# Optimization experiments

Hardware: AMD Instinct MI355X
Metric: run time of the kernel (lower is better)

Reference implementation:

```python
import jax, jax.numpy as jnp
import numpy as np

PRESERVE_RATIO = 0.8
TEMPERATURE = 1.5


def setup_inputs() -> dict:
    key = jax.random.key(0)
    ks = jax.random.split(key, 8)
    B, C, H, W = 2, 64, 96, 96
    inter = C // 2
    bott = C // 4
    s = 0.02
    return {
        "x": jax.random.normal(ks[0], (B, C, H, W), dtype=jnp.float32),
        "g_w": jax.random.normal(ks[1], (inter, C), dtype=jnp.float32) * s,
        "theta_w": jax.random.normal(ks[2], (inter, C), dtype=jnp.float32) * s,
        "phi_w": jax.random.normal(ks[3], (inter, C), dtype=jnp.float32) * s,
        "W_w": jax.random.normal(ks[4], (C, inter), dtype=jnp.float32) * s,
        "cg1_w": jax.random.normal(ks[5], (bott, C), dtype=jnp.float32) * s,
        "cg1_b": jnp.zeros((bott,), dtype=jnp.float32),
        "cg2_w": jax.random.normal(ks[6], (C, bott), dtype=jnp.float32) * s,
        "cg2_b": jnp.zeros((C,), dtype=jnp.float32),
    }


def reference(x, g_w, theta_w, phi_w, W_w, cg1_w, cg1_b, cg2_w, cg2_b):
    B, C, H, W = x.shape
    N = H * W
    # color gate: global avg pool -> 1x1 conv -> relu -> 1x1 conv -> sigmoid
    pooled = jnp.mean(x, axis=(2, 3))                       # [B, C]
    h = jax.nn.relu(pooled @ cg1_w.T + cg1_b)               # [B, C//4]
    gate = jax.nn.sigmoid(h @ cg2_w.T + cg2_b)              # [B, C]

    xf = x.reshape(B, C, N)                                 # [B, C, N]
    g_x = jnp.einsum('ic,bcn->bni', g_w, xf)                # [B, N, I]
    theta = jnp.einsum('ic,bcn->bni', theta_w, xf)          # [B, N, I]
    phi = jnp.einsum('ic,bcn->bin', phi_w, xf)              # [B, I, N]

    affinity = jnp.einsum('bni,bim->bnm', theta, phi) / TEMPERATURE  # [B, N, N]
    affinity = jax.nn.softmax(affinity, axis=-1)
    y = jnp.einsum('bnm,bmi->bni', affinity, g_x)           # [B, N, I]
    y = jnp.einsum('ci,bni->bcn', W_w, y).reshape(B, C, H, W)
    y = y * gate[:, :, None, None] * PRESERVE_RATIO
    return x + y
```

## Files before the change

kernel.cpp:

```cpp
#include <hip/hip_runtime.h>

#define N_TOK 9216
#define C_DIM 64
#define I_DIM 32
#define BOT 16
#define B_SZ 2
#define N_TILES 144

typedef short bf16x8 __attribute__((ext_vector_type(8)));
typedef float f32x4 __attribute__((ext_vector_type(4)));
typedef float f32x16 __attribute__((ext_vector_type(16)));

#define KST 40
#define VST 72

__device__ __forceinline__ unsigned packbf(float a, float b) {
  return __builtin_amdgcn_perm(__float_as_uint(b), __float_as_uint(a), 0x07060302u);
}
__device__ __forceinline__ unsigned short bftrunc(float f) {
  return (unsigned short)(__float_as_uint(f) >> 16);
}
__device__ __forceinline__ float bflo(unsigned u) { return __uint_as_float(u << 16); }
__device__ __forceinline__ float bfhi(unsigned u) { return __uint_as_float(u & 0xffff0000u); }

__global__ __launch_bounds__(256) void proj_pool_kernel(
    const float* __restrict__ x, const float* __restrict__ g_w,
    const float* __restrict__ theta_w, const float* __restrict__ phi_w,
    unsigned short* __restrict__ Q, unsigned short* __restrict__ K,
    unsigned short* __restrict__ VT, float* __restrict__ pooled) {
  if (blockIdx.x >= 216) {
    int bc = blockIdx.x - 216;
    const float* p = x + (size_t)bc * N_TOK;
    float s = 0.f;
    for (int t = threadIdx.x; t < N_TOK; t += 256) s += p[t];
#pragma unroll
    for (int off = 32; off >= 1; off >>= 1) s += __shfl_down(s, off, 64);
    __shared__ float red[4];
    int wid = threadIdx.x >> 6, lane = threadIdx.x & 63;
    if (lane == 0) red[wid] = s;
    __syncthreads();
    if (threadIdx.x == 0)
      pooled[bc] = (red[0] + red[1] + red[2] + red[3]) * (1.0f / N_TOK);
    return;
  }
  const int lane = threadIdx.x & 63;
  const int m = lane & 15, quad = lane >> 4;
  int task = blockIdx.x * 4 + (threadIdx.x >> 6);
  int mat = task / 288;
  int r0 = task % 288;
  int b = r0 / 144;
  int n0 = (r0 % 144) * 64;
  const float* wsrc = (mat == 0) ? theta_w : ((mat == 1) ? phi_w : g_w);
  const float scale = (mat == 0) ? 0.96179669439f : 1.0f;

  bf16x8 afr[2][2];
#pragma unroll
  for (int it = 0; it < 2; ++it)
#pragma unroll
    for (int cs = 0; cs < 2; ++cs) {
      const float* wp = wsrc + (it * 16 + m) * C_DIM + cs * 32 + quad * 8;
      union { unsigned u[4]; bf16x8 v; } t;
#pragma unroll
      for (int j = 0; j < 4; ++j)
        t.u[j] = packbf(wp[2 * j] * scale, wp[2 * j + 1] * scale);
      afr[it][cs] = t.v;
    }

#pragma unroll
  for (int sub = 0; sub < 4; ++sub) {
    const int ns = n0 + sub * 16;
    const float* xb = x + (size_t)b * C_DIM * N_TOK + ns + m;
    bf16x8 bfr[2];
#pragma unroll
    for (int cs = 0; cs < 2; ++cs) {
      union { unsigned u[4]; bf16x8 v; } t;
#pragma unroll
      for (int j = 0; j < 4; ++j) {
        float v0 = xb[(size_t)(cs * 32 + quad * 8 + 2 * j) * N_TOK];
        float v1 = xb[(size_t)(cs * 32 + quad * 8 + 2 * j + 1) * N_TOK];
        t.u[j] = packbf(v0, v1);
      }
      bfr[cs] = t.v;
    }

    f32x4 acc[2] = {{0.f, 0.f, 0.f, 0.f}, {0.f, 0.f, 0.f, 0.f}};
#pragma unroll
    for (int cs = 0; cs < 2; ++cs)
#pragma unroll
      for (int it = 0; it < 2; ++it)
        acc[it] = __builtin_amdgcn_mfma_f32_16x16x32_bf16(afr[it][cs], bfr[cs],
                                                          acc[it], 0, 0, 0);
    if (mat < 2) {
      unsigned short* dst =
          ((mat == 0) ? Q : K) + ((size_t)b * N_TOK + ns + m) * I_DIM;
#pragma unroll
      for (int it = 0; it < 2; ++it) {
        unsigned u0 = packbf(acc[it][0], acc[it][1]);
        unsigned u1 = packbf(acc[it][2], acc[it][3]);
        *(uint2*)(dst + it * 16 + quad * 4) = make_uint2(u0, u1);
      }
    } else {
#pragma unroll
      for (int it = 0; it < 2; ++it)
#pragma unroll
        for (int r = 0; r < 4; ++r)
          VT[((size_t)b * I_DIM + it * 16 + quad * 4 + r) * N_TOK + ns + m] =
              bftrunc(acc[it][r]);
    }
  }
}

__device__ __forceinline__ void tilework(const f32x16 s, const bf16x8 bvA,
                                         const bf16x8 bvB, f32x16& accy,
                                         float& lsum) {
  float e[16];
#pragma unroll
  for (int r = 0; r < 16; ++r) e[r] = __builtin_amdgcn_exp2f(s[r]);
  float l0 = 0.f, l1 = 0.f, l2 = 0.f, l3 = 0.f;
#pragma unroll
  for (int r = 0; r < 4; ++r) {
    l0 += e[r]; l1 += e[4 + r]; l2 += e[8 + r]; l3 += e[12 + r];
  }
  lsum += (l0 + l1) + (l2 + l3);
  unsigned pk[8];
#pragma unroll
  for (int i = 0; i < 8; ++i) pk[i] = packbf(e[2 * i], e[2 * i + 1]);
  asm("v_permlane32_swap_b32 %0, %1" : "+v"(pk[0]), "+v"(pk[2]));
  asm("v_permlane32_swap_b32 %0, %1" : "+v"(pk[1]), "+v"(pk[3]));
  asm("v_permlane32_swap_b32 %0, %1" : "+v"(pk[4]), "+v"(pk[6]));
  asm("v_permlane32_swap_b32 %0, %1" : "+v"(pk[5]), "+v"(pk[7]));
  union { unsigned u[4]; bf16x8 v; } A0, A1;
  A0.u[0] = pk[0]; A0.u[1] = pk[1]; A0.u[2] = pk[2]; A0.u[3] = pk[3];
  A1.u[0] = pk[4]; A1.u[1] = pk[5]; A1.u[2] = pk[6]; A1.u[3] = pk[7];
  accy = __builtin_amdgcn_mfma_f32_32x32x16_bf16(A0.v, bvA, accy, 0, 0, 0);
  accy = __builtin_amdgcn_mfma_f32_32x32x16_bf16(A1.v, bvB, accy, 0, 0, 0);
}

__global__ __launch_bounds__(256, 4) void attn_kernel(
    const unsigned short* __restrict__ Q, const unsigned short* __restrict__ Kg,
    const unsigned short* __restrict__ VT, unsigned short* __restrict__ Ypart,
    float* __restrict__ Lpart, int tps) {
  const int tid = threadIdx.x;
  const int lane = tid & 63;
  const int l32 = lane & 31, h = lane >> 5;
  const int ks = blockIdx.y, b = blockIdx.z;
  const int q0 = blockIdx.x * 128 + (tid >> 6) * 32;
  const unsigned short* Qb = Q + (size_t)b * N_TOK * I_DIM;
  const unsigned short* Kb = Kg + (size_t)b * N_TOK * I_DIM;
  const unsigned short* Vb = VT + (size_t)b * I_DIM * N_TOK;

  __shared__ __align__(16) unsigned short Ks[2][64 * KST];
  __shared__ __align__(16) unsigned short Vs[2][32 * VST];

  bf16x8 bq0 = *(const bf16x8*)(Qb + (size_t)(q0 + l32) * I_DIM + h * 8);
  bf16x8 bq1 = *(const bf16x8*)(Qb + (size_t)(q0 + l32) * I_DIM + 16 + h * 8);

  f32x16 accy = {};
  float lsum = 0.f;
  const f32x16 zz = {};

  const int kt0 = ks * tps;
  const int kr = tid >> 2, kc = (tid & 3) * 8;
  const int vr = tid >> 3, vc = (tid & 7) * 8;
  const unsigned short* kgp = Kb + ((size_t)kt0 * 64 + kr) * I_DIM + kc;
  const unsigned short* vgp = Vb + (size_t)vr * N_TOK + kt0 * 64 + vc;

  {
    uint4 r0k = *(const uint4*)kgp;
    uint4 r0v = *(const uint4*)vgp;
    *(uint4*)&Ks[0][kr * KST + kc] = r0k;
    *(uint4*)&Vs[0][vr * VST + vc] = r0v;
  }
  uint4 rk = {0, 0, 0, 0}, rv = {0, 0, 0, 0};
  if (tps > 1) {
    rk = *(const uint4*)(kgp + 64 * I_DIM);
    rv = *(const uint4*)(vgp + 64);
  }
  __syncthreads();

  for (int kt = 0; kt < tps; ++kt) {
    const int p = kt & 1;
    uint4 rk2 = {0, 0, 0, 0}, rv2 = {0, 0, 0, 0};
    if (kt + 2 < tps) {
      rk2 = *(const uint4*)(kgp + (size_t)(kt + 2) * 64 * I_DIM);
      rv2 = *(const uint4*)(vgp + (kt + 2) * 64);
    }
    asm volatile("" ::: "memory");

    bf16x8 ak00 = *(const bf16x8*)&Ks[p][l32 * KST + 8 * h];
    bf16x8 ak01 = *(const bf16x8*)&Ks[p][l32 * KST + 16 + 8 * h];
    bf16x8 ak10 = *(const bf16x8*)&Ks[p][(32 + l32) * KST + 8 * h];
    bf16x8 ak11 = *(const bf16x8*)&Ks[p][(32 + l32) * KST + 16 + 8 * h];
    bf16x8 bv0 = *(const bf16x8*)&Vs[p][l32 * VST + 8 * h];
    bf16x8 bv1 = *(const bf16x8*)&Vs[p][l32 * VST + 16 + 8 * h];
    bf16x8 bv2 = *(const bf16x8*)&Vs[p][l32 * VST + 32 + 8 * h];
    bf16x8 bv3 = *(const bf16x8*)&Vs[p][l32 * VST + 48 + 8 * h];

    f32x16 s0 = __builtin_amdgcn_mfma_f32_32x32x16_bf16(ak00, bq0, zz, 0, 0, 0);
    s0 = __builtin_amdgcn_mfma_f32_32x32x16_bf16(ak01, bq1, s0, 0, 0, 0);
    f32x16 s1 = __builtin_amdgcn_mfma_f32_32x32x16_bf16(ak10, bq0, zz, 0, 0, 0);
    s1 = __builtin_amdgcn_mfma_f32_32x32x16_bf16(ak11, bq1, s1, 0, 0, 0);

    tilework(s0, bv0, bv1, accy, lsum);
    tilework(s1, bv2, bv3, accy, lsum);

    if (kt + 1 < tps) {
      *(uint4*)&Ks[1 - p][kr * KST + kc] = rk;
      *(uint4*)&Vs[1 - p][vr * VST + vc] = rv;
    }
    rk = rk2; rv = rv2;
    __syncthreads();
  }

  lsum += __shfl_xor(lsum, 32, 64);

  const size_t base = (size_t)(ks * B_SZ + b) * N_TOK + q0;
#pragma unroll
  for (int R = 0; R < 4; ++R)
#pragma unroll
    for (int r = 0; r < 4; ++r)
      Ypart[(base + r + 8 * R + 4 * h) * I_DIM + l32] = bftrunc(accy[4 * R + r]);
  if (h == 0) Lpart[base + l32] = lsum;
}

__global__ __launch_bounds__(256) void epilogue_kernel(
    const float* __restrict__ x, const float* __restrict__ W_w,
    const float* __restrict__ pooled, const float* __restrict__ cg1_w,
    const float* __restrict__ cg1_b, const float* __restrict__ cg2_w,
    const float* __restrict__ cg2_b, const unsigned short* __restrict__ Ypart,
    const float* __restrict__ Lpart, float* __restrict__ out, int KS) {
  __shared__ float Ysh[64][33];
  __shared__ float lsh[64];
  __shared__ float gsh[64];
  __shared__ float hl[BOT];
  const int t = threadIdx.x;
  const int b = blockIdx.y;
  const int n0 = blockIdx.x * 64;

  if (t < BOT) {
    float a = cg1_b[t];
#pragma unroll
    for (int c = 0; c < C_DIM; ++c)
      a += cg1_w[t * C_DIM + c] * pooled[b * C_DIM + c];
    hl[t] = a > 0.f ? a : 0.f;
  }

  {
    int nl = t >> 2, i0 = (t & 3) * 8;
    float s[8];
#pragma unroll
    for (int k = 0; k < 8; ++k) s[k] = 0.f;
    for (int ks = 0; ks < KS; ++ks) {
      const unsigned short* yp =
          Ypart + ((size_t)(ks * B_SZ + b) * N_TOK + n0 + nl) * I_DIM + i0;
      uint4 v = *(const uint4*)yp;
      s[0] += bflo(v.x); s[1] += bfhi(v.x);
      s[2] += bflo(v.y); s[3] += bfhi(v.y);
      s[4] += bflo(v.z); s[5] += bfhi(v.z);
      s[6] += bflo(v.w); s[7] += bfhi(v.w);
    }
#pragma unroll
    for (int k = 0; k < 8; ++k) Ysh[nl][i0 + k] = s[k];
    if (t < 64) {
      float ls = 0.f;
      for (int ks = 0; ks < KS; ++ks)
        ls += Lpart[(size_t)(ks * B_SZ + b) * N_TOK + n0 + t];
      lsh[t] = ls;
    }
  }
  __syncthreads();

  if (t < C_DIM) {
    float z = cg2_b[t];
#pragma unroll
    for (int j = 0; j < BOT; ++j) z += cg2_w[t * BOT + j] * hl[j];
    gsh[t] = 0.8f / (1.f + __expf(-z));
  }
  __syncthreads();

  const int n = t & 63, cg = t >> 6;
  float y[I_DIM];
#pragma unroll
  for (int i = 0; i < I_DIM; ++i) y[i] = Ysh[n][i];
  const float inv = 1.0f / lsh[n];
  const float* xb = x + ((size_t)b * C_DIM + cg * 16) * N_TOK + n0 + n;
  float* ob = out + ((size_t)b * C_DIM + cg * 16) * N_TOK + n0 + n;
#pragma unroll
  for (int c16 = 0; c16 < 16; ++c16) {
    const int c = cg * 16 + c16;
    float sacc = 0.f;
#pragma unroll
    for (int i = 0; i < I_DIM; ++i) sacc += W_w[c * I_DIM + i] * y[i];
    ob[(size_t)c16 * N_TOK] = xb[(size_t)c16 * N_TOK] + gsh[c] * inv * sacc;
  }
}

extern "C" void kernel_launch(void* const* d_in, const int* in_sizes, int n_in,
                              void* d_out, int out_size, void* d_ws, size_t ws_size,
                              hipStream_t stream) {
  const float* x = (const float*)d_in[0];
  const float* g_w = (const float*)d_in[1];
  const float* theta_w = (const float*)d_in[2];
  const float* phi_w = (const float*)d_in[3];
  const float* W_w = (const float*)d_in[4];
  const float* cg1_w = (const float*)d_in[5];
  const float* cg1_b = (const float*)d_in[6];
  const float* cg2_w = (const float*)d_in[7];
  const float* cg2_b = (const float*)d_in[8];
  float* out = (float*)d_out;

  char* w = (char*)d_ws;
  const size_t bfsz = (size_t)B_SZ * N_TOK * I_DIM * sizeof(unsigned short);
  unsigned short* Qb = (unsigned short*)(w);
  unsigned short* Kb = (unsigned short*)(w + bfsz);
  unsigned short* VT = (unsigned short*)(w + 2 * bfsz);
  float* pooled = (float*)(w + 3 * bfsz);
  char* w2 = w + 3 * bfsz + 8192;

  int KS = 16;
  {
    const size_t per = (size_t)B_SZ * N_TOK * (I_DIM * 2 + 4);
    while (KS > 1 && (3 * bfsz + 8192 + (size_t)KS * per) > ws_size) KS >>= 1;
  }
  float* Lpart = (float*)w2;
  unsigned short* Ypart =
      (unsigned short*)(w2 + (size_t)KS * B_SZ * N_TOK * sizeof(float));
  int tps = N_TILES / KS;

  proj_pool_kernel<<<dim3(344), 256, 0, stream>>>(x, g_w, theta_w, phi_w, Qb,
                                                  Kb, VT, pooled);
  attn_kernel<<<dim3(72, KS, B_SZ), 256, 0, stream>>>(Qb, Kb, VT, Ypart, Lpart, tps);
  epilogue_kernel<<<dim3(N_TOK / 64, B_SZ), 256, 0, stream>>>(
      x, W_w, pooled, cg1_w, cg1_b, cg2_w, cg2_b, Ypart, Lpart, out, KS);
}
```

Before: 147.0 us.

## Process two query groups per wave and single-buffer K/V tiles

Each wave now handles 64 queries (two 32-row groups) instead of 32, so every K/V tile loaded into shared memory and registers is reused across twice as many MFMA score/PV computations. Blocks shrink to 128 threads (2 waves), and the double-buffered shared tiles become single-buffered, with prefetch held in registers and two barriers per iteration. This lowers LDS traffic per query, but costs more registers (two accumulators, four Q fragments), lowers occupancy and adds a barrier per iteration.

```diff
diff --git a/kernel.cpp b/kernel.cpp
--- a/kernel.cpp
+++ b/kernel.cpp
@@ -136,7 +136,7 @@
   accy = __builtin_amdgcn_mfma_f32_32x32x16_bf16(A1.v, bvB, accy, 0, 0, 0);
 }
 
-__global__ __launch_bounds__(256, 4) void attn_kernel(
+__global__ __launch_bounds__(128, 2) void attn_kernel(
     const unsigned short* __restrict__ Q, const unsigned short* __restrict__ Kg,
     const unsigned short* __restrict__ VT, unsigned short* __restrict__ Ypart,
     float* __restrict__ Lpart, int tps) {
@@ -144,83 +144,101 @@
   const int lane = tid & 63;
   const int l32 = lane & 31, h = lane >> 5;
   const int ks = blockIdx.y, b = blockIdx.z;
-  const int q0 = blockIdx.x * 128 + (tid >> 6) * 32;
+  const int q0 = blockIdx.x * 128 + (tid >> 6) * 64;
   const unsigned short* Qb = Q + (size_t)b * N_TOK * I_DIM;
   const unsigned short* Kb = Kg + (size_t)b * N_TOK * I_DIM;
   const unsigned short* Vb = VT + (size_t)b * I_DIM * N_TOK;
 
-  __shared__ __align__(16) unsigned short Ks[2][64 * KST];
-  __shared__ __align__(16) unsigned short Vs[2][32 * VST];
-
-  bf16x8 bq0 = *(const bf16x8*)(Qb + (size_t)(q0 + l32) * I_DIM + h * 8);
-  bf16x8 bq1 = *(const bf16x8*)(Qb + (size_t)(q0 + l32) * I_DIM + 16 + h * 8);
-
-  f32x16 accy = {};
-  float lsum = 0.f;
+  __shared__ __align__(16) unsigned short Ks[64 * KST];
+  __shared__ __align__(16) unsigned short Vs[32 * VST];
+
+  bf16x8 bq[4];
+#pragma unroll
+  for (int qg = 0; qg < 2; ++qg) {
+    bq[2 * qg] = *(const bf16x8*)(Qb + (size_t)(q0 + qg * 32 + l32) * I_DIM + h * 8);
+    bq[2 * qg + 1] =
+        *(const bf16x8*)(Qb + (size_t)(q0 + qg * 32 + l32) * I_DIM + 16 + h * 8);
+  }
+
+  f32x16 accy[2] = {{}, {}};
+  float lsum[2] = {0.f, 0.f};
   const f32x16 zz = {};
 
   const int kt0 = ks * tps;
-  const int kr = tid >> 2, kc = (tid & 3) * 8;
-  const int vr = tid >> 3, vc = (tid & 7) * 8;
+  const int kr = tid >> 1, kc = (tid & 1) * 16;
+  const int vr = tid >> 2, vc = (tid & 3) * 16;
   const unsigned short* kgp = Kb + ((size_t)kt0 * 64 + kr) * I_DIM + kc;
   const unsigned short* vgp = Vb + (size_t)vr * N_TOK + kt0 * 64 + vc;
+  unsigned short* klp = &Ks[kr * KST + kc];
+  unsigned short* vlp = &Vs[vr * VST + vc];
 
   {
-    uint4 r0k = *(const uint4*)kgp;
-    uint4 r0v = *(const uint4*)vgp;
-    *(uint4*)&Ks[0][kr * KST + kc] = r0k;
-    *(uint4*)&Vs[0][vr * VST + vc] = r0v;
-  }
-  uint4 rk = {0, 0, 0, 0}, rv = {0, 0, 0, 0};
-  if (tps > 1) {
-    rk = *(const uint4*)(kgp + 64 * I_DIM);
-    rv = *(const uint4*)(vgp + 64);
-  }
-  __syncthreads();
+    uint4 k0a = *(const uint4*)kgp;
+    uint4 k0b = *(const uint4*)(kgp + 8);
+    uint4 v0a = *(const uint4*)vgp;
+    uint4 v0b = *(const uint4*)(vgp + 8);
+    *(uint4*)(klp) = k0a;
+    *(uint4*)(klp + 8) = k0b;
+    *(uint4*)(vlp) = v0a;
+    *(uint4*)(vlp + 8) = v0b;
+  }
 
   for (int kt = 0; kt < tps; ++kt) {
-    const int p = kt & 1;
-    uint4 rk2 = {0, 0, 0, 0}, rv2 = {0, 0, 0, 0};
-    if (kt + 2 < tps) {
-      rk2 = *(const uint4*)(kgp + (size_t)(kt + 2) * 64 * I_DIM);
-      rv2 = *(const uint4*)(vgp + (kt + 2) * 64);
+    __syncthreads();
+    const bool pf = (kt + 1 < tps);
+    uint4 rka = {0, 0, 0, 0}, rkb = rka, rva = rka, rvb = rka;
+    if (pf) {
+      const unsigned short* kn = kgp + (size_t)(kt + 1) * 64 * I_DIM;
+      const unsigned short* vn = vgp + (kt + 1) * 64;
+      rka = *(const uint4*)kn;
+      rkb = *(const uint4*)(kn + 8);
+      rva = *(const uint4*)vn;
+      rvb = *(const uint4*)(vn + 8);
     }
     asm volatile("" ::: "memory");
 
-    bf16x8 ak00 = *(const bf16x8*)&Ks[p][l32 * KST + 8 * h];
-    bf16x8 ak01 = *(const bf16x8*)&Ks[p][l32 * KST + 16 + 8 * h];
-    bf16x8 ak10 = *(const bf16x8*)&Ks[p][(32 + l32) * KST + 8 * h];
-    bf16x8 ak11 = *(const bf16x8*)&Ks[p][(32 + l32) * KST + 16 + 8 * h];
-    bf16x8 bv0 = *(const bf16x8*)&Vs[p][l32 * VST + 8 * h];
-    bf16x8 bv1 = *(const bf16x8*)&Vs[p][l32 * VST + 16 + 8 * h];
-    bf16x8 bv2 = *(const bf16x8*)&Vs[p][l32 * VST + 32 + 8 * h];
-    bf16x8 bv3 = *(const bf16x8*)&Vs[p][l32 * VST + 48 + 8 * h];
-
-    f32x16 s0 = __builtin_amdgcn_mfma_f32_32x32x16_bf16(ak00, bq0, zz, 0, 0, 0);
-    s0 = __builtin_amdgcn_mfma_f32_32x32x16_bf16(ak01, bq1, s0, 0, 0, 0);
-    f32x16 s1 = __builtin_amdgcn_mfma_f32_32x32x16_bf16(ak10, bq0, zz, 0, 0, 0);
-    s1 = __builtin_amdgcn_mfma_f32_32x32x16_bf16(ak11, bq1, s1, 0, 0, 0);
-
-    tilework(s0, bv0, bv1, accy, lsum);
-    tilework(s1, bv2, bv3, accy, lsum);
-
-    if (kt + 1 < tps) {
-      *(uint4*)&Ks[1 - p][kr * KST + kc] = rk;
-      *(uint4*)&Vs[1 - p][vr * VST + vc] = rv;
-    }
-    rk = rk2; rv = rv2;
+    bf16x8 ak00 = *(const bf16x8*)&Ks[l32 * KST + 8 * h];
+    bf16x8 ak01 = *(const bf16x8*)&Ks[l32 * KST + 16 + 8 * h];
+    bf16x8 ak10 = *(const bf16x8*)&Ks[(32 + l32) * KST + 8 * h];
+    bf16x8 ak11 = *(const bf16x8*)&Ks[(32 + l32) * KST + 16 + 8 * h];
+    bf16x8 bv0 = *(const bf16x8*)&Vs[l32 * VST + 8 * h];
+    bf16x8 bv1 = *(const bf16x8*)&Vs[l32 * VST + 16 + 8 * h];
+    bf16x8 bv2 = *(const bf16x8*)&Vs[l32 * VST + 32 + 8 * h];
+    bf16x8 bv3 = *(const bf16x8*)&Vs[l32 * VST + 48 + 8 * h];
+
+#pragma unroll
+    for (int qg = 0; qg < 2; ++qg) {
+      f32x16 s0 = __builtin_amdgcn_mfma_f32_32x32x16_bf16(ak00, bq[2 * qg], zz, 0, 0, 0);
+      s0 = __builtin_amdgcn_mfma_f32_32x32x16_bf16(ak01, bq[2 * qg + 1], s0, 0, 0, 0);
+      f32x16 s1 = __builtin_amdgcn_mfma_f32_32x32x16_bf16(ak10, bq[2 * qg], zz, 0, 0, 0);
+      s1 = __builtin_amdgcn_mfma_f32_32x32x16_bf16(ak11, bq[2 * qg + 1], s1, 0, 0, 0);
+      tilework(s0, bv0, bv1, accy[qg], lsum[qg]);
+      tilework(s1, bv2, bv3, accy[qg], lsum[qg]);
+    }
+
     __syncthreads();
-  }
-
-  lsum += __shfl_xor(lsum, 32, 64);
+    if (pf) {
+      *(uint4*)(klp) = rka;
+      *(uint4*)(klp + 8) = rkb;
+      *(uint4*)(vlp) = rva;
+      *(uint4*)(vlp + 8) = rvb;
+    }
+  }
+
+#pragma unroll
+  for (int qg = 0; qg < 2; ++qg) lsum[qg] += __shfl_xor(lsum[qg], 32, 64);
 
   const size_t base = (size_t)(ks * B_SZ + b) * N_TOK + q0;
 #pragma unroll
-  for (int R = 0; R < 4; ++R)
-#pragma unroll
-    for (int r = 0; r < 4; ++r)
-      Ypart[(base + r + 8 * R + 4 * h) * I_DIM + l32] = bftrunc(accy[4 * R + r]);
-  if (h == 0) Lpart[base + l32] = lsum;
+  for (int qg = 0; qg < 2; ++qg) {
+#pragma unroll
+    for (int R = 0; R < 4; ++R)
+#pragma unroll
+      for (int r = 0; r < 4; ++r)
+        Ypart[(base + qg * 32 + r + 8 * R + 4 * h) * I_DIM + l32] =
+            bftrunc(accy[qg][4 * R + r]);
+    if (h == 0) Lpart[base + qg * 32 + l32] = lsum[qg];
+  }
 }
 
 __global__ __launch_bounds__(256) void epilogue_kernel(
@@ -329,7 +347,7 @@
 
   proj_pool_kernel<<<dim3(344), 256, 0, stream>>>(x, g_w, theta_w, phi_w, Qb,
                                                   Kb, VT, pooled);
-  attn_kernel<<<dim3(72, KS, B_SZ), 256, 0, stream>>>(Qb, Kb, VT, Ypart, Lpart, tps);
+  attn_kernel<<<dim3(72, KS, B_SZ), 128, 0, stream>>>(Qb, Kb, VT, Ypart, Lpart, tps);
   epilogue_kernel<<<dim3(N_TOK / 64, B_SZ), 256, 0, stream>>>(
       x, W_w, pooled, cg1_w, cg1_b, cg2_w, cg2_b, Ypart, Lpart, out, KS);
 }
```

Result: slower. 150.2 us (+2.2%).

## Fuse epilogue into attention via last-block counter, merge QKV projections, single-buffer LDS

Applied to the files above, without the earlier changes.

The epilogue kernel is removed. Its work now runs inside the attention kernel: the last key-split block to finish for each query tile, detected through an atomic counter that the projection kernel zeroes, does the reduction. The projection kernel now computes theta, phi and g together per task, so x is read once instead of three times, and it launches fewer blocks. The attention K/V staging changes from double-buffered LDS to a single buffer with register prefetch and two barriers per tile, which saves shared memory but may expose more latency. The aim is to cut one launch and repeated x reads, at the cost of serialized tail work in the last blocks.

```diff
diff --git a/kernel.cpp b/kernel.cpp
--- a/kernel.cpp
+++ b/kernel.cpp
@@ -27,9 +27,10 @@
     const float* __restrict__ x, const float* __restrict__ g_w,
     const float* __restrict__ theta_w, const float* __restrict__ phi_w,
     unsigned short* __restrict__ Q, unsigned short* __restrict__ K,
-    unsigned short* __restrict__ VT, float* __restrict__ pooled) {
-  if (blockIdx.x >= 216) {
-    int bc = blockIdx.x - 216;
+    unsigned short* __restrict__ VT, float* __restrict__ pooled,
+    int* __restrict__ cnt) {
+  if (blockIdx.x >= 72) {
+    int bc = blockIdx.x - 72;
     const float* p = x + (size_t)bc * N_TOK;
     float s = 0.f;
     for (int t = threadIdx.x; t < N_TOK; t += 256) s += p[t];
@@ -43,28 +44,31 @@
       pooled[bc] = (red[0] + red[1] + red[2] + red[3]) * (1.0f / N_TOK);
     return;
   }
+  if (blockIdx.x == 0 && threadIdx.x < 72 * B_SZ) cnt[threadIdx.x] = 0;
+
   const int lane = threadIdx.x & 63;
   const int m = lane & 15, quad = lane >> 4;
   int task = blockIdx.x * 4 + (threadIdx.x >> 6);
-  int mat = task / 288;
-  int r0 = task % 288;
-  int b = r0 / 144;
-  int n0 = (r0 % 144) * 64;
-  const float* wsrc = (mat == 0) ? theta_w : ((mat == 1) ? phi_w : g_w);
-  const float scale = (mat == 0) ? 0.96179669439f : 1.0f;
-
-  bf16x8 afr[2][2];
-#pragma unroll
-  for (int it = 0; it < 2; ++it)
-#pragma unroll
-    for (int cs = 0; cs < 2; ++cs) {
-      const float* wp = wsrc + (it * 16 + m) * C_DIM + cs * 32 + quad * 8;
-      union { unsigned u[4]; bf16x8 v; } t;
-#pragma unroll
-      for (int j = 0; j < 4; ++j)
-        t.u[j] = packbf(wp[2 * j] * scale, wp[2 * j + 1] * scale);
-      afr[it][cs] = t.v;
-    }
+  int b = task / 144;
+  int n0 = (task % 144) * 64;
+
+  bf16x8 afr[3][2][2];
+#pragma unroll
+  for (int m3 = 0; m3 < 3; ++m3) {
+    const float* wsrc = (m3 == 0) ? theta_w : ((m3 == 1) ? phi_w : g_w);
+    const float scale = (m3 == 0) ? 0.96179669439f : 1.0f;
+#pragma unroll
+    for (int it = 0; it < 2; ++it)
+#pragma unroll
+      for (int cs = 0; cs < 2; ++cs) {
+        const float* wp = wsrc + (it * 16 + m) * C_DIM + cs * 32 + quad * 8;
+        union { unsigned u[4]; bf16x8 v; } t;
+#pragma unroll
+        for (int j = 0; j < 4; ++j)
+          t.u[j] = packbf(wp[2 * j] * scale, wp[2 * j + 1] * scale);
+        afr[m3][it][cs] = t.v;
+      }
+  }
 
 #pragma unroll
   for (int sub = 0; sub < 4; ++sub) {
@@ -83,30 +87,37 @@
       bfr[cs] = t.v;
     }
 
-    f32x4 acc[2] = {{0.f, 0.f, 0.f, 0.f}, {0.f, 0.f, 0.f, 0.f}};
+    f32x4 acc[3][2];
+#pragma unroll
+    for (int m3 = 0; m3 < 3; ++m3)
+#pragma unroll
+      for (int it = 0; it < 2; ++it) acc[m3][it] = (f32x4){0.f, 0.f, 0.f, 0.f};
 #pragma unroll
     for (int cs = 0; cs < 2; ++cs)
 #pragma unroll
-      for (int it = 0; it < 2; ++it)
-        acc[it] = __builtin_amdgcn_mfma_f32_16x16x32_bf16(afr[it][cs], bfr[cs],
-                                                          acc[it], 0, 0, 0);
-    if (mat < 2) {
+      for (int m3 = 0; m3 < 3; ++m3)
+#pragma unroll
+        for (int it = 0; it < 2; ++it)
+          acc[m3][it] = __builtin_amdgcn_mfma_f32_16x16x32_bf16(
+              afr[m3][it][cs], bfr[cs], acc[m3][it], 0, 0, 0);
+
+#pragma unroll
+    for (int m3 = 0; m3 < 2; ++m3) {
       unsigned short* dst =
-          ((mat == 0) ? Q : K) + ((size_t)b * N_TOK + ns + m) * I_DIM;
+          ((m3 == 0) ? Q : K) + ((size_t)b * N_TOK + ns + m) * I_DIM;
 #pragma unroll
       for (int it = 0; it < 2; ++it) {
-        unsigned u0 = packbf(acc[it][0], acc[it][1]);
-        unsigned u1 = packbf(acc[it][2], acc[it][3]);
+        unsigned u0 = packbf(acc[m3][it][0], acc[m3][it][1]);
+        unsigned u1 = packbf(acc[m3][it][2], acc[m3][it][3]);
         *(uint2*)(dst + it * 16 + quad * 4) = make_uint2(u0, u1);
       }
-    } else {
-#pragma unroll
-      for (int it = 0; it < 2; ++it)
-#pragma unroll
-        for (int r = 0; r < 4; ++r)
-          VT[((size_t)b * I_DIM + it * 16 + quad * 4 + r) * N_TOK + ns + m] =
-              bftrunc(acc[it][r]);
-    }
+    }
+#pragma unroll
+    for (int it = 0; it < 2; ++it)
+#pragma unroll
+      for (int r = 0; r < 4; ++r)
+        VT[((size_t)b * I_DIM + it * 16 + quad * 4 + r) * N_TOK + ns + m] =
+            bftrunc(acc[2][it][r]);
   }
 }
 
@@ -139,18 +150,25 @@
 __global__ __launch_bounds__(256, 4) void attn_kernel(
     const unsigned short* __restrict__ Q, const unsigned short* __restrict__ Kg,
     const unsigned short* __restrict__ VT, unsigned short* __restrict__ Ypart,
-    float* __restrict__ Lpart, int tps) {
+    float* __restrict__ Lpart, const float* __restrict__ x,
+    const float* __restrict__ W_w, const float* __restrict__ pooled,
+    const float* __restrict__ cg1_w, const float* __restrict__ cg1_b,
+    const float* __restrict__ cg2_w, const float* __restrict__ cg2_b,
+    float* __restrict__ out, int* __restrict__ cnt, int KS, int tps) {
+  __shared__ __align__(16) char smem[17728];
+  __shared__ int sLast;
+  unsigned short* Ks = (unsigned short*)smem;
+  unsigned short* Vs = (unsigned short*)(smem + 5120);
+
   const int tid = threadIdx.x;
   const int lane = tid & 63;
   const int l32 = lane & 31, h = lane >> 5;
+  const int qb = blockIdx.x;
   const int ks = blockIdx.y, b = blockIdx.z;
-  const int q0 = blockIdx.x * 128 + (tid >> 6) * 32;
+  const int q0 = qb * 128 + (tid >> 6) * 32;
   const unsigned short* Qb = Q + (size_t)b * N_TOK * I_DIM;
   const unsigned short* Kb = Kg + (size_t)b * N_TOK * I_DIM;
   const unsigned short* Vb = VT + (size_t)b * I_DIM * N_TOK;
-
-  __shared__ __align__(16) unsigned short Ks[2][64 * KST];
-  __shared__ __align__(16) unsigned short Vs[2][32 * VST];
 
   bf16x8 bq0 = *(const bf16x8*)(Qb + (size_t)(q0 + l32) * I_DIM + h * 8);
   bf16x8 bq1 = *(const bf16x8*)(Qb + (size_t)(q0 + l32) * I_DIM + 16 + h * 8);
@@ -164,37 +182,34 @@
   const int vr = tid >> 3, vc = (tid & 7) * 8;
   const unsigned short* kgp = Kb + ((size_t)kt0 * 64 + kr) * I_DIM + kc;
   const unsigned short* vgp = Vb + (size_t)vr * N_TOK + kt0 * 64 + vc;
+  unsigned short* klp = &Ks[kr * KST + kc];
+  unsigned short* vlp = &Vs[vr * VST + vc];
 
   {
-    uint4 r0k = *(const uint4*)kgp;
-    uint4 r0v = *(const uint4*)vgp;
-    *(uint4*)&Ks[0][kr * KST + kc] = r0k;
-    *(uint4*)&Vs[0][vr * VST + vc] = r0v;
-  }
-  uint4 rk = {0, 0, 0, 0}, rv = {0, 0, 0, 0};
-  if (tps > 1) {
-    rk = *(const uint4*)(kgp + 64 * I_DIM);
-    rv = *(const uint4*)(vgp + 64);
-  }
-  __syncthreads();
+    uint4 rk = *(const uint4*)kgp;
+    uint4 rv = *(const uint4*)vgp;
+    *(uint4*)klp = rk;
+    *(uint4*)vlp = rv;
+  }
 
   for (int kt = 0; kt < tps; ++kt) {
-    const int p = kt & 1;
-    uint4 rk2 = {0, 0, 0, 0}, rv2 = {0, 0, 0, 0};
-    if (kt + 2 < tps) {
-      rk2 = *(const uint4*)(kgp + (size_t)(kt + 2) * 64 * I_DIM);
-      rv2 = *(const uint4*)(vgp + (kt + 2) * 64);
+    __syncthreads();
+    const bool pf = (kt + 1 < tps);
+    uint4 rk = {0, 0, 0, 0}, rv = {0, 0, 0, 0};
+    if (pf) {
+      rk = *(const uint4*)(kgp + (size_t)(kt + 1) * 64 * I_DIM);
+      rv = *(const uint4*)(vgp + (kt + 1) * 64);
     }
     asm volatile("" ::: "memory");
 
-    bf16x8 ak00 = *(const bf16x8*)&Ks[p][l32 * KST + 8 * h];
-    bf16x8 ak01 = *(const bf16x8*)&Ks[p][l32 * KST + 16 + 8 * h];
-    bf16x8 ak10 = *(const bf16x8*)&Ks[p][(32 + l32) * KST + 8 * h];
-    bf16x8 ak11 = *(const bf16x8*)&Ks[p][(32 + l32) * KST + 16 + 8 * h];
-    bf16x8 bv0 = *(const bf16x8*)&Vs[p][l32 * VST + 8 * h];
-    bf16x8 bv1 = *(const bf16x8*)&Vs[p][l32 * VST + 16 + 8 * h];
-    bf16x8 bv2 = *(const bf16x8*)&Vs[p][l32 * VST + 32 + 8 * h];
-    bf16x8 bv3 = *(const bf16x8*)&Vs[p][l32 * VST + 48 + 8 * h];
+    bf16x8 ak00 = *(const bf16x8*)&Ks[l32 * KST + 8 * h];
+    bf16x8 ak01 = *(const bf16x8*)&Ks[l32 * KST + 16 + 8 * h];
+    bf16x8 ak10 = *(const bf16x8*)&Ks[(32 + l32) * KST + 8 * h];
+    bf16x8 ak11 = *(const bf16x8*)&Ks[(32 + l32) * KST + 16 + 8 * h];
+    bf16x8 bv0 = *(const bf16x8*)&Vs[l32 * VST + 8 * h];
+    bf16x8 bv1 = *(const bf16x8*)&Vs[l32 * VST + 16 + 8 * h];
+    bf16x8 bv2 = *(const bf16x8*)&Vs[l32 * VST + 32 + 8 * h];
+    bf16x8 bv3 = *(const bf16x8*)&Vs[l32 * VST + 48 + 8 * h];
 
     f32x16 s0 = __builtin_amdgcn_mfma_f32_32x32x16_bf16(ak00, bq0, zz, 0, 0, 0);
     s0 = __builtin_amdgcn_mfma_f32_32x32x16_bf16(ak01, bq1, s0, 0, 0, 0);
@@ -204,12 +219,11 @@
     tilework(s0, bv0, bv1, accy, lsum);
     tilework(s1, bv2, bv3, accy, lsum);
 
-    if (kt + 1 < tps) {
-      *(uint4*)&Ks[1 - p][kr * KST + kc] = rk;
-      *(uint4*)&Vs[1 - p][vr * VST + vc] = rv;
-    }
-    rk = rk2; rv = rv2;
     __syncthreads();
+    if (pf) {
+      *(uint4*)klp = rk;
+      *(uint4*)vlp = rv;
+    }
   }
 
   lsum += __shfl_xor(lsum, 32, 64);
@@ -221,77 +235,78 @@
     for (int r = 0; r < 4; ++r)
       Ypart[(base + r + 8 * R + 4 * h) * I_DIM + l32] = bftrunc(accy[4 * R + r]);
   if (h == 0) Lpart[base + l32] = lsum;
-}
-
-__global__ __launch_bounds__(256) void epilogue_kernel(
-    const float* __restrict__ x, const float* __restrict__ W_w,
-    const float* __restrict__ pooled, const float* __restrict__ cg1_w,
-    const float* __restrict__ cg1_b, const float* __restrict__ cg2_w,
-    const float* __restrict__ cg2_b, const unsigned short* __restrict__ Ypart,
-    const float* __restrict__ Lpart, float* __restrict__ out, int KS) {
-  __shared__ float Ysh[64][33];
-  __shared__ float lsh[64];
-  __shared__ float gsh[64];
-  __shared__ float hl[BOT];
-  const int t = threadIdx.x;
-  const int b = blockIdx.y;
-  const int n0 = blockIdx.x * 64;
-
-  if (t < BOT) {
-    float a = cg1_b[t];
-#pragma unroll
-    for (int c = 0; c < C_DIM; ++c)
-      a += cg1_w[t * C_DIM + c] * pooled[b * C_DIM + c];
-    hl[t] = a > 0.f ? a : 0.f;
-  }
+
+  __threadfence();
+  __syncthreads();
+  if (tid == 0) sLast = (atomicAdd(&cnt[b * 72 + qb], 1) == KS - 1);
+  __syncthreads();
+  if (!sLast) return;
+  __threadfence();
+
+  float(*Ysh)[33] = (float(*)[33])smem;
+  float* lsh = (float*)(smem + 16896);
+  float* gsh = (float*)(smem + 17408);
+  float* hl = (float*)(smem + 17664);
+  const int n0e = qb * 128;
 
   {
-    int nl = t >> 2, i0 = (t & 3) * 8;
-    float s[8];
-#pragma unroll
-    for (int k = 0; k < 8; ++k) s[k] = 0.f;
-    for (int ks = 0; ks < KS; ++ks) {
+    const int nl = tid >> 1, i0 = (tid & 1) * 16;
+    float s[16];
+#pragma unroll
+    for (int k = 0; k < 16; ++k) s[k] = 0.f;
+    for (int kr2 = 0; kr2 < KS; ++kr2) {
       const unsigned short* yp =
-          Ypart + ((size_t)(ks * B_SZ + b) * N_TOK + n0 + nl) * I_DIM + i0;
-      uint4 v = *(const uint4*)yp;
-      s[0] += bflo(v.x); s[1] += bfhi(v.x);
-      s[2] += bflo(v.y); s[3] += bfhi(v.y);
-      s[4] += bflo(v.z); s[5] += bfhi(v.z);
-      s[6] += bflo(v.w); s[7] += bfhi(v.w);
-    }
-#pragma unroll
-    for (int k = 0; k < 8; ++k) Ysh[nl][i0 + k] = s[k];
-    if (t < 64) {
+          Ypart + ((size_t)(kr2 * B_SZ + b) * N_TOK + n0e + nl) * I_DIM + i0;
+      uint4 v0 = ((const uint4*)yp)[0];
+      uint4 v1 = ((const uint4*)yp)[1];
+      s[0] += bflo(v0.x); s[1] += bfhi(v0.x);
+      s[2] += bflo(v0.y); s[3] += bfhi(v0.y);
+      s[4] += bflo(v0.z); s[5] += bfhi(v0.z);
+      s[6] += bflo(v0.w); s[7] += bfhi(v0.w);
+      s[8] += bflo(v1.x); s[9] += bfhi(v1.x);
+      s[10] += bflo(v1.y); s[11] += bfhi(v1.y);
+      s[12] += bflo(v1.z); s[13] += bfhi(v1.z);
+      s[14] += bflo(v1.w); s[15] += bfhi(v1.w);
+    }
+#pragma unroll
+    for (int k = 0; k < 16; ++k) Ysh[nl][i0 + k] = s[k];
+    if (tid < 128) {
       float ls = 0.f;
-      for (int ks = 0; ks < KS; ++ks)
-        ls += Lpart[(size_t)(ks * B_SZ + b) * N_TOK + n0 + t];
-      lsh[t] = ls;
+      for (int kr2 = 0; kr2 < KS; ++kr2)
+        ls += Lpart[(size_t)(kr2 * B_SZ + b) * N_TOK + n0e + tid];
+      lsh[tid] = ls;
+    }
+    if (tid < BOT) {
+      float a = cg1_b[tid];
+#pragma unroll
+      for (int c = 0; c < C_DIM; ++c)
+        a += cg1_w[tid * C_DIM + c] * pooled[b * C_DIM + c];
+      hl[tid] = a > 0.f ? a : 0.f;
     }
   }
   __syncthreads();
-
-  if (t < C_DIM) {
-    float z = cg2_b[t];
-#pragma unroll
-    for (int j = 0; j < BOT; ++j) z += cg2_w[t * BOT + j] * hl[j];
-    gsh[t] = 0.8f / (1.f + __expf(-z));
+  if (tid < C_DIM) {
+    float z = cg2_b[tid];
+#pragma unroll
+    for (int j = 0; j < BOT; ++j) z += cg2_w[tid * BOT + j] * hl[j];
+    gsh[tid] = 0.8f / (1.f + __expf(-z));
   }
   __syncthreads();
 
-  const int n = t & 63, cg = t >> 6;
+  const int n = tid & 127, cgp = tid >> 7;
   float y[I_DIM];
 #pragma unroll
   for (int i = 0; i < I_DIM; ++i) y[i] = Ysh[n][i];
   const float inv = 1.0f / lsh[n];
-  const float* xb = x + ((size_t)b * C_DIM + cg * 16) * N_TOK + n0 + n;
-  float* ob = out + ((size_t)b * C_DIM + cg * 16) * N_TOK + n0 + n;
-#pragma unroll
-  for (int c16 = 0; c16 < 16; ++c16) {
-    const int c = cg * 16 + c16;
+  const float* xb2 = x + ((size_t)b * C_DIM + cgp * 32) * N_TOK + n0e + n;
+  float* ob = out + ((size_t)b * C_DIM + cgp * 32) * N_TOK + n0e + n;
+#pragma unroll
+  for (int c32 = 0; c32 < 32; ++c32) {
+    const int c = cgp * 32 + c32;
     float sacc = 0.f;
 #pragma unroll
     for (int i = 0; i < I_DIM; ++i) sacc += W_w[c * I_DIM + i] * y[i];
-    ob[(size_t)c16 * N_TOK] = xb[(size_t)c16 * N_TOK] + gsh[c] * inv * sacc;
+    ob[(size_t)c32 * N_TOK] = xb2[(size_t)c32 * N_TOK] + gsh[c] * inv * sacc;
   }
 }
 
@@ -315,6 +330,7 @@
   unsigned short* Kb = (unsigned short*)(w + bfsz);
   unsigned short* VT = (unsigned short*)(w + 2 * bfsz);
   float* pooled = (float*)(w + 3 * bfsz);
+  int* cnt = (int*)(w + 3 * bfsz + 1024);
   char* w2 = w + 3 * bfsz + 8192;
 
   int KS = 16;
@@ -327,9 +343,9 @@
       (unsigned short*)(w2 + (size_t)KS * B_SZ * N_TOK * sizeof(float));
   int tps = N_TILES / KS;
 
-  proj_pool_kernel<<<dim3(344), 256, 0, stream>>>(x, g_w, theta_w, phi_w, Qb,
-                                                  Kb, VT, pooled);
-  attn_kernel<<<dim3(72, KS, B_SZ), 256, 0, stream>>>(Qb, Kb, VT, Ypart, Lpart, tps);
-  epilogue_kernel<<<dim3(N_TOK / 64, B_SZ), 256, 0, stream>>>(
-      x, W_w, pooled, cg1_w, cg1_b, cg2_w, cg2_b, Ypart, Lpart, out, KS);
-}
+  proj_pool_kernel<<<dim3(200), 256, 0, stream>>>(x, g_w, theta_w, phi_w, Qb,
+                                                  Kb, VT, pooled, cnt);
+  attn_kernel<<<dim3(72, KS, B_SZ), 256, 0, stream>>>(
+      Qb, Kb, VT, Ypart, Lpart, x, W_w, pooled, cg1_w, cg1_b, cg2_w, cg2_b,
+      out, cnt, KS, tps);
+}
```

Result: slower. 382.6 us (+160.4%).
